# Optimization experiments

Measured on AMD Instinct MI355X. Metric: run time of the kernel, lower is better.

The kernel has to match this reference:

```python
import jax, jax.numpy as jnp
import numpy as np

D_MODEL = 1024
N_HEADS = 16
D_H = D_MODEL // N_HEADS
B, T = 4, 2048
NEG_INF = jnp.finfo(jnp.float32).min


def setup_inputs() -> dict:
    key = jax.random.key(0)
    ks = jax.random.split(key, 9)
    s = 1.0 / np.sqrt(D_MODEL)
    inp = {
        "x": jax.random.normal(ks[0], (B, T, D_MODEL), dtype=jnp.float32),
        "pad_mask": jnp.zeros((B, T), dtype=bool),
        "Wq": jax.random.uniform(ks[1], (D_MODEL, D_MODEL), jnp.float32, -s, s),
        "bq": jax.random.uniform(ks[2], (D_MODEL,), jnp.float32, -s, s),
        "Wk": jax.random.uniform(ks[3], (D_MODEL, D_MODEL), jnp.float32, -s, s),
        "bk": jax.random.uniform(ks[4], (D_MODEL,), jnp.float32, -s, s),
        "Wv": jax.random.uniform(ks[5], (D_MODEL, D_MODEL), jnp.float32, -s, s),
        "bv": jax.random.uniform(ks[6], (D_MODEL,), jnp.float32, -s, s),
        "Wo": jax.random.uniform(ks[7], (D_MODEL, D_MODEL), jnp.float32, -s, s),
        "bo": jax.random.uniform(ks[8], (D_MODEL,), jnp.float32, -s, s),
    }
    return inp


def reference(x, pad_mask, Wq, bq, Wk, bk, Wv, bv, Wo, bo):
    b, t, _ = x.shape
    # torch Linear: y = x @ W.T + b
    def proj(W, bias):
        y = jnp.einsum("btd,ed->bte", x, W) + bias
        return y.reshape(b, t, N_HEADS, D_H).transpose(0, 2, 1, 3)  # (B,H,T,d_h)

    Q, K, V = proj(Wq, bq), proj(Wk, bk), proj(Wv, bv)
    S = jnp.einsum("bhqd,bhkd->bhqk", Q, K) / jnp.sqrt(jnp.float32(D_H))
    causal = jnp.triu(jnp.ones((t, t), dtype=bool), k=1)[None, None]
    S = jnp.where(causal, NEG_INF, S)
    S = jnp.where(pad_mask[:, None, None, :], NEG_INF, S)
    A = jax.nn.softmax(S, axis=-1)
    Y = jnp.einsum("bhqk,bhkd->bhqd", A, V)
    Y = Y.transpose(0, 2, 1, 3).reshape(b, t, D_MODEL)
    O = jnp.einsum("btd,ed->bte", Y, Wo) + bo
    return O
```

## Files before the change

### kernel.cpp

```cpp
#include <hip/hip_runtime.h>
#include <stdint.h>
#include <stddef.h>

#define Tq 2048
#define DM 1024

typedef unsigned short u16;
typedef __bf16 bf16x8 __attribute__((ext_vector_type(8)));
typedef float f32x4 __attribute__((ext_vector_type(4)));
typedef unsigned short u16x8 __attribute__((ext_vector_type(8)));
typedef unsigned short u16x4 __attribute__((ext_vector_type(4)));

__device__ __forceinline__ float bf2f(u16 h) {
    union { unsigned int u; float f; } c; c.u = ((unsigned int)h) << 16; return c.f;
}
__device__ __forceinline__ u16 f2bf(float f) {
    union { float f; unsigned int u; } c; c.f = f;
    unsigned int u = c.u;
    return (u16)((u + 0x7fffu + ((u >> 16) & 1u)) >> 16);
}

#define GLD(gp, lp) __builtin_amdgcn_global_load_lds(                                  \
        (const __attribute__((address_space(1))) void*)(gp),                           \
        (__attribute__((address_space(3))) void*)(lp), 16, 0, 0)

__device__ __forceinline__ int sniff_fp32(const u16* xs) {
    const int lane = threadIdx.x & 63;
    const u16 u = xs[lane];
    const int e = (u >> 7) & 0xFF;
    unsigned long long m = __ballot(e >= 160);
    return __popcll(m) >= 4;
}

__device__ __forceinline__ void cvt_body(const void* src, u16* dst, int i0, int fmt) {
    if (fmt) {
        const float* s = (const float*)src;
        float4 a = *(const float4*)(s + i0);
        float4 b = *(const float4*)(s + i0 + 4);
        u16x8 o;
        o[0] = f2bf(a.x); o[1] = f2bf(a.y); o[2] = f2bf(a.z); o[3] = f2bf(a.w);
        o[4] = f2bf(b.x); o[5] = f2bf(b.y); o[6] = f2bf(b.z); o[7] = f2bf(b.w);
        *(u16x8*)(dst + i0) = o;
    } else {
        *(u16x8*)(dst + i0) = *(const u16x8*)((const u16*)src + i0);
    }
}

__global__ void cvt_tensor(const void* __restrict__ src, u16* __restrict__ dst, int n,
                           const u16* __restrict__ xs, int* flag, int writeflag) {
    const int fmt = sniff_fp32(xs);
    if (writeflag && blockIdx.x == 0 && threadIdx.x == 0) *flag = fmt;
    const int i0 = (blockIdx.x * 256 + threadIdx.x) * 8;
    if (i0 >= n) return;
    cvt_body(src, dst, i0, fmt);
}

__global__ void cvt_w4b(const void* s0, const void* s1, const void* s2, const void* s3,
                        const void* t0, const void* t1, const void* t2, const void* t3,
                        u16* __restrict__ dstW, float* __restrict__ dstB,
                        const u16* __restrict__ xs) {
    const int fmt = sniff_fp32(xs);
    const int wsel = blockIdx.y;
    const void* s = (wsel == 0) ? s0 : (wsel == 1) ? s1 : (wsel == 2) ? s2 : s3;
    u16* d = dstW + (size_t)wsel * (DM * DM);
    const int i0 = (blockIdx.x * 256 + threadIdx.x) * 8;
    cvt_body(s, d, i0, fmt);
    if (blockIdx.x == 0) {
        const void* bs = (wsel == 0) ? t0 : (wsel == 1) ? t1 : (wsel == 2) ? t2 : t3;
        float* db = dstB + (size_t)wsel * DM;
        const int j0 = threadIdx.x * 4;
        if (fmt) {
            *(float4*)(db + j0) = *(const float4*)((const float*)bs + j0);
        } else {
            const u16* ss = (const u16*)bs;
            db[j0+0] = bf2f(ss[j0+0]); db[j0+1] = bf2f(ss[j0+1]);
            db[j0+2] = bf2f(ss[j0+2]); db[j0+3] = bf2f(ss[j0+3]);
        }
    }
}

__global__ __launch_bounds__(256, 2) void gemm_bt(
    const u16* __restrict__ A,
    const u16* __restrict__ W0, const u16* __restrict__ W1, const u16* __restrict__ W2,
    const float* __restrict__ b0, const float* __restrict__ b1, const float* __restrict__ b2,
    u16* o0, u16* o1, u16* o2,
    const int* __restrict__ flag, int mode)
{
    __shared__ u16 Alds[128 * 64];
    __shared__ u16 Blds[128 * 64];

    const int K = DM;
    const int i = blockIdx.x;
    const int j = blockIdx.y;
    const int which = (mode == 0) ? (j >> 3) : 0;
    const u16* W      = (which == 0) ? W0 : (which == 1) ? W1 : W2;
    const float* bias = (which == 0) ? b0 : (which == 1) ? b1 : b2;
    u16* out          = (which == 0) ? o0 : (which == 1) ? o1 : o2;
    const int jn = (mode == 0) ? (j & 7) : j;
    const int m0 = i * 128, n0 = jn * 128;
    const int ofmt = (mode == 1) ? *flag : 0;

    const int tid = threadIdx.x;
    const int w = tid >> 6, lane = tid & 63;
    const int l4 = lane & 15, quad = lane >> 4;
    const int wrow = w >> 1, wcol = w & 1;

    f32x4 acc[4][4] = {};

    for (int k0 = 0; k0 < K; k0 += 64) {
        __syncthreads();
#pragma unroll
        for (int c = 0; c < 4; ++c) {
            const int u   = w * 1024 + c * 4096;
            const int off = u + lane * 16;
            const int row = off >> 7;
            const int col = (off & 127) >> 1;
            GLD(A + (size_t)(m0 + row) * K + k0 + col, (char*)Alds + u);
            GLD(W + (size_t)(n0 + row) * K + k0 + col, (char*)Blds + u);
        }
        __syncthreads();
#pragma unroll
        for (int c = 0; c < 2; ++c) {
            bf16x8 af[4], bfr[4];
#pragma unroll
            for (int r = 0; r < 4; ++r)
                af[r] = *(const bf16x8*)&Alds[(wrow*64 + r*16 + l4) * 64 + c*32 + quad*8];
#pragma unroll
            for (int n = 0; n < 4; ++n)
                bfr[n] = *(const bf16x8*)&Blds[(wcol*64 + n*16 + l4) * 64 + c*32 + quad*8];
#pragma unroll
            for (int r = 0; r < 4; ++r)
#pragma unroll
                for (int n = 0; n < 4; ++n)
                    acc[r][n] = __builtin_amdgcn_mfma_f32_16x16x32_bf16(af[r], bfr[n], acc[r][n], 0, 0, 0);
        }
    }

#pragma unroll
    for (int n = 0; n < 4; ++n) {
        const int col = n0 + wcol*64 + n*16 + l4;
        const float bv = bias[col];
#pragma unroll
        for (int r = 0; r < 4; ++r) {
            const int mb = m0 + wrow*64 + r*16 + quad*4;
            if (mode == 0 && which == 2) {
                const int b = mb >> 11, t0 = mb & 2047;
                const int h = col >> 6, d = col & 63;
                u16x4 pk;
#pragma unroll
                for (int reg = 0; reg < 4; ++reg) pk[reg] = f2bf(acc[r][n][reg] + bv);
                *(u16x4*)&out[((size_t)(b*16 + h) * 64 + d) * 2048 + t0] = pk;
            } else {
#pragma unroll
                for (int reg = 0; reg < 4; ++reg) {
                    const int m = mb + reg;
                    const float val = acc[r][n][reg] + bv;
                    if (mode == 0) {
                        const int b = m >> 11, t = m & 2047;
                        const int h = col >> 6, d = col & 63;
                        out[(size_t)((b*16 + h) * 2048 + t) * 64 + d] = f2bf(val);
                    } else if (ofmt) {
                        ((float*)out)[(size_t)m * DM + col] = val;
                    } else {
                        out[(size_t)m * DM + col] = f2bf(val);
                    }
                }
            }
        }
    }
}

#define LSTR 72

__global__ __launch_bounds__(256, 2) void attn4(
    const u16* __restrict__ Qb, const u16* __restrict__ Kb, const u16* __restrict__ VT,
    const unsigned char* __restrict__ pad,
    u16* __restrict__ Y)
{
    __shared__ u16 Klds[64 * LSTR];
    __shared__ u16 Vtl [64 * LSTR];
    __shared__ u16 Pl  [4][64 * LSTR];
    __shared__ unsigned char padl[64];

    const int nb = blockIdx.y;
    const int bh = blockIdx.x;
    const int b = bh >> 4, h = bh & 15;
    const u16* Qp  = Qb + (size_t)bh * (Tq * 64);
    const u16* Kp  = Kb + (size_t)bh * (Tq * 64);
    const u16* VTp = VT + (size_t)bh * (64 * Tq);

    const int tid = threadIdx.x;
    const int w = tid >> 6, lane = tid & 63;
    const int l4 = lane & 15, quad = lane >> 4;

    const int qt[4] = { nb, nb + 8, 23 - nb, 31 - nb };

    bf16x8 qf[4][2];
#pragma unroll
    for (int g = 0; g < 4; ++g) {
        const u16* r = Qp + (size_t)(qt[g] * 64 + w * 16 + l4) * 64 + quad * 8;
        qf[g][0] = *(const bf16x8*)r;
        qf[g][1] = *(const bf16x8*)(r + 32);
    }

    f32x4 o[4][4] = {};
    float l[4][4] = {};

    const int srow = tid >> 2;
    const int sc   = (tid & 3) * 16;

    u16x8 kr0, kr1, vr0, vr1; unsigned char pr = 0;
    {
        const u16* kg = Kp + (size_t)srow * 64 + sc;
        kr0 = *(const u16x8*)kg; kr1 = *(const u16x8*)(kg + 8);
        const u16* vg = VTp + (size_t)srow * Tq + sc;
        vr0 = *(const u16x8*)vg; vr1 = *(const u16x8*)(vg + 8);
        if (tid < 64) pr = pad[(size_t)b * Tq + tid];
    }

    const float SC = 0.18033688011112042f;
    const int ktmax = qt[3];

    for (int kt = 0; kt <= ktmax; ++kt) {
        const int k0 = kt * 64;
        __syncthreads();
        *(u16x8*)&Klds[srow * LSTR + sc]     = kr0;
        *(u16x8*)&Klds[srow * LSTR + sc + 8] = kr1;
        *(u16x8*)&Vtl [srow * LSTR + sc]     = vr0;
        *(u16x8*)&Vtl [srow * LSTR + sc + 8] = vr1;
        if (tid < 64) padl[tid] = pr;
        __syncthreads();
        if (kt < ktmax) {
            const u16* kg = Kp + (size_t)(k0 + 64 + srow) * 64 + sc;
            kr0 = *(const u16x8*)kg; kr1 = *(const u16x8*)(kg + 8);
            const u16* vg = VTp + (size_t)srow * Tq + k0 + 64 + sc;
            vr0 = *(const u16x8*)vg; vr1 = *(const u16x8*)(vg + 8);
            if (tid < 64) pr = pad[(size_t)b * Tq + k0 + 64 + tid];
        }

        const bool anypad = __any((int)(padl[lane] != 0));

        bf16x8 kf[2][4];
#pragma unroll
        for (int c = 0; c < 2; ++c)
#pragma unroll
            for (int n = 0; n < 4; ++n)
                kf[c][n] = *(const bf16x8*)&Klds[(n * 16 + l4) * LSTR + c * 32 + quad * 8];

#pragma unroll
        for (int g = 0; g < 4; ++g) {
            if (kt > qt[g]) continue;
            f32x4 sacc[4] = {};
            __builtin_amdgcn_s_setprio(1);
#pragma unroll
            for (int c = 0; c < 2; ++c)
#pragma unroll
                for (int n = 0; n < 4; ++n)
                    sacc[n] = __builtin_amdgcn_mfma_f32_16x16x32_bf16(qf[g][c], kf[c][n], sacc[n], 0, 0, 0);
            __builtin_amdgcn_s_setprio(0);
            u16* Pg = &Pl[g][0];
            if (kt == qt[g] || anypad) {
                bool pm[4];
#pragma unroll
                for (int n = 0; n < 4; ++n) pm[n] = (padl[n * 16 + l4] != 0);
                const int qr = qt[g] * 64 + w * 16 + quad * 4;
#pragma unroll
                for (int r = 0; r < 4; ++r) {
                    float rs = 0.f;
#pragma unroll
                    for (int n = 0; n < 4; ++n) {
                        const int kgi = k0 + n * 16 + l4;
                        const bool msk = (kgi > qr + r) || pm[n];
                        const float p = msk ? 0.0f : exp2f(sacc[n][r] * SC);
                        rs += p;
                        *(__bf16*)&Pg[(w * 16 + quad * 4 + r) * LSTR + n * 16 + l4] = (__bf16)p;
                    }
                    l[g][r] += rs;
                }
            } else {
#pragma unroll
                for (int r = 0; r < 4; ++r) {
                    float rs = 0.f;
#pragma unroll
                    for (int n = 0; n < 4; ++n) {
                        const float p = exp2f(sacc[n][r] * SC);
                        rs += p;
                        *(__bf16*)&Pg[(w * 16 + quad * 4 + r) * LSTR + n * 16 + l4] = (__bf16)p;
                    }
                    l[g][r] += rs;
                }
            }
        }

        bf16x8 vf[2][4];
#pragma unroll
        for (int c = 0; c < 2; ++c)
#pragma unroll
            for (int t = 0; t < 4; ++t)
                vf[c][t] = *(const bf16x8*)&Vtl[(t * 16 + l4) * LSTR + c * 32 + quad * 8];

#pragma unroll
        for (int g = 0; g < 4; ++g) {
            if (kt > qt[g]) continue;
            __builtin_amdgcn_s_setprio(1);
#pragma unroll
            for (int c = 0; c < 2; ++c) {
                bf16x8 pf = *(const bf16x8*)&Pl[g][(w * 16 + l4) * LSTR + c * 32 + quad * 8];
#pragma unroll
                for (int t = 0; t < 4; ++t)
                    o[g][t] = __builtin_amdgcn_mfma_f32_16x16x32_bf16(pf, vf[c][t], o[g][t], 0, 0, 0);
            }
            __builtin_amdgcn_s_setprio(0);
        }
    }

#pragma unroll
    for (int g = 0; g < 4; ++g)
#pragma unroll
        for (int r = 0; r < 4; ++r)
#pragma unroll
            for (int s = 1; s < 16; s <<= 1)
                l[g][r] += __shfl_xor(l[g][r], s);

#pragma unroll
    for (int g = 0; g < 4; ++g)
#pragma unroll
        for (int r = 0; r < 4; ++r) {
            const float inv = 1.0f / l[g][r];
            u16* y = Y + (size_t)(b * Tq + (qt[g] * 64 + w * 16 + quad * 4 + r)) * DM + h * 64;
#pragma unroll
            for (int t = 0; t < 4; ++t)
                *(__bf16*)&y[t * 16 + l4] = (__bf16)(o[g][t][r] * inv);
        }
}

extern "C" void kernel_launch(void* const* d_in, const int* in_sizes, int n_in,
                              void* d_out, int out_size, void* d_ws, size_t ws_size,
                              hipStream_t stream) {
    const void* x  = d_in[0];
    const unsigned char* pad = (const unsigned char*)d_in[1];
    const void* Wq = d_in[2];
    const void* bq = d_in[3];
    const void* Wk = d_in[4];
    const void* bk = d_in[5];
    const void* Wv = d_in[6];
    const void* bv = d_in[7];
    const void* Wo = d_in[8];
    const void* bo = d_in[9];
    const u16* xs = (const u16*)x;

    const size_t NEL = (size_t)8192 * 1024;
    const size_t WEL = (size_t)1024 * 1024;

    int* flag   = (int*)d_ws;
    u16* base16 = (u16*)((char*)d_ws + 256);
    u16* xc     = base16;
    u16* Wc     = base16 + NEL;
    float* bf_  = (float*)(base16 + NEL + 4*WEL);
    u16* Qb     = (u16*)(bf_ + 4096);
    u16* Kb     = Qb + NEL;
    u16* VT     = Kb + NEL;
    u16* Yb     = xc;

    cvt_tensor<<<dim3((int)(NEL/2048)), 256, 0, stream>>>(x, xc, (int)NEL, xs, flag, 1);
    cvt_w4b<<<dim3(512, 4), 256, 0, stream>>>(Wq, Wk, Wv, Wo, bq, bk, bv, bo, Wc, bf_, xs);

    gemm_bt<<<dim3(64, 24), 256, 0, stream>>>(xc, Wc, Wc + WEL, Wc + 2*WEL,
                                              bf_, bf_ + 1024, bf_ + 2048,
                                              Qb, Kb, VT, flag, 0);
    attn4<<<dim3(64, 8), 256, 0, stream>>>(Qb, Kb, VT, pad, Yb);
    gemm_bt<<<dim3(64, 8), 256, 0, stream>>>(Yb, Wc + 3*WEL, Wc + 3*WEL, Wc + 3*WEL,
                                             bf_ + 3072, bf_ + 3072, bf_ + 3072,
                                             (u16*)d_out, nullptr, nullptr, flag, 1);
}
```

Before: 282.0 us.

## Double-buffer K/V tiles in attention and merge conversion kernels into one launch

The attention kernel now keeps two LDS buffers for K, V^T and the pad mask. The next tile is written into the alternate buffer at the end of each iteration, which removes one __syncthreads per key tile. The separate activation and weight conversion kernels are merged into a single launch to cut launch overhead. The extra LDS (about 18 KB more per block) may lower occupancy at 2 blocks per CU.

Result: no change. 278.1 us (-1.4%).

```diff
diff --git a/kernel.cpp b/kernel.cpp
--- a/kernel.cpp
+++ b/kernel.cpp
@@ -46,35 +46,36 @@
     }
 }
 
-__global__ void cvt_tensor(const void* __restrict__ src, u16* __restrict__ dst, int n,
-                           const u16* __restrict__ xs, int* flag, int writeflag) {
+__global__ void cvt_all(const void* __restrict__ x,
+                        const void* s0, const void* s1, const void* s2, const void* s3,
+                        const void* t0, const void* t1, const void* t2, const void* t3,
+                        u16* __restrict__ xc, u16* __restrict__ dstW, float* __restrict__ dstB,
+                        const u16* __restrict__ xs, int* flag) {
     const int fmt = sniff_fp32(xs);
-    if (writeflag && blockIdx.x == 0 && threadIdx.x == 0) *flag = fmt;
-    const int i0 = (blockIdx.x * 256 + threadIdx.x) * 8;
-    if (i0 >= n) return;
-    cvt_body(src, dst, i0, fmt);
-}
-
-__global__ void cvt_w4b(const void* s0, const void* s1, const void* s2, const void* s3,
-                        const void* t0, const void* t1, const void* t2, const void* t3,
-                        u16* __restrict__ dstW, float* __restrict__ dstB,
-                        const u16* __restrict__ xs) {
-    const int fmt = sniff_fp32(xs);
-    const int wsel = blockIdx.y;
-    const void* s = (wsel == 0) ? s0 : (wsel == 1) ? s1 : (wsel == 2) ? s2 : s3;
-    u16* d = dstW + (size_t)wsel * (DM * DM);
-    const int i0 = (blockIdx.x * 256 + threadIdx.x) * 8;
-    cvt_body(s, d, i0, fmt);
-    if (blockIdx.x == 0) {
-        const void* bs = (wsel == 0) ? t0 : (wsel == 1) ? t1 : (wsel == 2) ? t2 : t3;
-        float* db = dstB + (size_t)wsel * DM;
-        const int j0 = threadIdx.x * 4;
-        if (fmt) {
-            *(float4*)(db + j0) = *(const float4*)((const float*)bs + j0);
-        } else {
-            const u16* ss = (const u16*)bs;
-            db[j0+0] = bf2f(ss[j0+0]); db[j0+1] = bf2f(ss[j0+1]);
-            db[j0+2] = bf2f(ss[j0+2]); db[j0+3] = bf2f(ss[j0+3]);
+    int bx = blockIdx.x;
+    if (bx < 4096) {
+        if (bx == 0 && threadIdx.x == 0) *flag = fmt;
+        const int i0 = (bx * 256 + threadIdx.x) * 8;
+        cvt_body(x, xc, i0, fmt);
+    } else {
+        bx -= 4096;
+        const int wsel = bx >> 9;
+        const int bi   = bx & 511;
+        const void* s = (wsel == 0) ? s0 : (wsel == 1) ? s1 : (wsel == 2) ? s2 : s3;
+        u16* d = dstW + (size_t)wsel * (DM * DM);
+        const int i0 = (bi * 256 + threadIdx.x) * 8;
+        cvt_body(s, d, i0, fmt);
+        if (bi == 0) {
+            const void* bs = (wsel == 0) ? t0 : (wsel == 1) ? t1 : (wsel == 2) ? t2 : t3;
+            float* db = dstB + (size_t)wsel * DM;
+            const int j0 = threadIdx.x * 4;
+            if (fmt) {
+                *(float4*)(db + j0) = *(const float4*)((const float*)bs + j0);
+            } else {
+                const u16* ss = (const u16*)bs;
+                db[j0+0] = bf2f(ss[j0+0]); db[j0+1] = bf2f(ss[j0+1]);
+                db[j0+2] = bf2f(ss[j0+2]); db[j0+3] = bf2f(ss[j0+3]);
+            }
         }
     }
 }
@@ -177,10 +178,10 @@
     const unsigned char* __restrict__ pad,
     u16* __restrict__ Y)
 {
-    __shared__ u16 Klds[64 * LSTR];
-    __shared__ u16 Vtl [64 * LSTR];
+    __shared__ u16 Klds[2][64 * LSTR];
+    __shared__ u16 Vtl [2][64 * LSTR];
     __shared__ u16 Pl  [4][64 * LSTR];
-    __shared__ unsigned char padl[64];
+    __shared__ unsigned char padl[2][64];
 
     const int nb = blockIdx.y;
     const int bh = blockIdx.x;
@@ -217,18 +218,18 @@
         vr0 = *(const u16x8*)vg; vr1 = *(const u16x8*)(vg + 8);
         if (tid < 64) pr = pad[(size_t)b * Tq + tid];
     }
+    *(u16x8*)&Klds[0][srow * LSTR + sc]     = kr0;
+    *(u16x8*)&Klds[0][srow * LSTR + sc + 8] = kr1;
+    *(u16x8*)&Vtl [0][srow * LSTR + sc]     = vr0;
+    *(u16x8*)&Vtl [0][srow * LSTR + sc + 8] = vr1;
+    if (tid < 64) padl[0][tid] = pr;
 
     const float SC = 0.18033688011112042f;
     const int ktmax = qt[3];
 
     for (int kt = 0; kt <= ktmax; ++kt) {
+        const int cur = kt & 1;
         const int k0 = kt * 64;
-        __syncthreads();
-        *(u16x8*)&Klds[srow * LSTR + sc]     = kr0;
-        *(u16x8*)&Klds[srow * LSTR + sc + 8] = kr1;
-        *(u16x8*)&Vtl [srow * LSTR + sc]     = vr0;
-        *(u16x8*)&Vtl [srow * LSTR + sc + 8] = vr1;
-        if (tid < 64) padl[tid] = pr;
         __syncthreads();
         if (kt < ktmax) {
             const u16* kg = Kp + (size_t)(k0 + 64 + srow) * 64 + sc;
@@ -238,14 +239,14 @@
             if (tid < 64) pr = pad[(size_t)b * Tq + k0 + 64 + tid];
         }
 
-        const bool anypad = __any((int)(padl[lane] != 0));
+        const bool anypad = __any((int)(padl[cur][lane] != 0));
 
         bf16x8 kf[2][4];
 #pragma unroll
         for (int c = 0; c < 2; ++c)
 #pragma unroll
             for (int n = 0; n < 4; ++n)
-                kf[c][n] = *(const bf16x8*)&Klds[(n * 16 + l4) * LSTR + c * 32 + quad * 8];
+                kf[c][n] = *(const bf16x8*)&Klds[cur][(n * 16 + l4) * LSTR + c * 32 + quad * 8];
 
 #pragma unroll
         for (int g = 0; g < 4; ++g) {
@@ -262,7 +263,7 @@
             if (kt == qt[g] || anypad) {
                 bool pm[4];
 #pragma unroll
-                for (int n = 0; n < 4; ++n) pm[n] = (padl[n * 16 + l4] != 0);
+                for (int n = 0; n < 4; ++n) pm[n] = (padl[cur][n * 16 + l4] != 0);
                 const int qr = qt[g] * 64 + w * 16 + quad * 4;
 #pragma unroll
                 for (int r = 0; r < 4; ++r) {
@@ -297,7 +298,7 @@
         for (int c = 0; c < 2; ++c)
 #pragma unroll
             for (int t = 0; t < 4; ++t)
-                vf[c][t] = *(const bf16x8*)&Vtl[(t * 16 + l4) * LSTR + c * 32 + quad * 8];
+                vf[c][t] = *(const bf16x8*)&Vtl[cur][(t * 16 + l4) * LSTR + c * 32 + quad * 8];
 
 #pragma unroll
         for (int g = 0; g < 4; ++g) {
@@ -311,6 +312,14 @@
                     o[g][t] = __builtin_amdgcn_mfma_f32_16x16x32_bf16(pf, vf[c][t], o[g][t], 0, 0, 0);
             }
             __builtin_amdgcn_s_setprio(0);
+        }
+
+        if (kt < ktmax) {
+            *(u16x8*)&Klds[cur ^ 1][srow * LSTR + sc]     = kr0;
+            *(u16x8*)&Klds[cur ^ 1][srow * LSTR + sc + 8] = kr1;
+            *(u16x8*)&Vtl [cur ^ 1][srow * LSTR + sc]     = vr0;
+            *(u16x8*)&Vtl [cur ^ 1][srow * LSTR + sc + 8] = vr1;
+            if (tid < 64) padl[cur ^ 1][tid] = pr;
         }
     }
 
@@ -362,8 +371,8 @@
     u16* VT     = Kb + NEL;
     u16* Yb     = xc;
 
-    cvt_tensor<<<dim3((int)(NEL/2048)), 256, 0, stream>>>(x, xc, (int)NEL, xs, flag, 1);
-    cvt_w4b<<<dim3(512, 4), 256, 0, stream>>>(Wq, Wk, Wv, Wo, bq, bk, bv, bo, Wc, bf_, xs);
+    cvt_all<<<dim3(6144), 256, 0, stream>>>(x, Wq, Wk, Wv, Wo, bq, bk, bv, bo,
+                                            xc, Wc, bf_, xs, flag);
 
     gemm_bt<<<dim3(64, 24), 256, 0, stream>>>(xc, Wc, Wc + WEL, Wc + 2*WEL,
                                               bf_, bf_ + 1024, bf_ + 2048,
```
